# Kernel tuning notes

Measured on AMD Instinct MI355X. Metric: run time of the kernel, lower is better.

Reference implementation:

```python
import jax, jax.numpy as jnp
import numpy as np

IMG_SIZE = 1536.0
NUM_ANCHORS = 145152  # 3*(48^2 + 96^2 + 192^2) for strides 32/16/8 at 1536px
NUM_CH = 85           # 4 box + 1 obj + 80 classes


def setup_inputs() -> dict:
    key = jax.random.key(0)
    k1, k2 = jax.random.split(key)
    predictions = jax.random.uniform(k1, (1, NUM_ANCHORS, NUM_CH), dtype=jnp.float32)
    score_threshold = jax.random.uniform(k2, (1,), dtype=jnp.float32)
    return {"predictions": predictions, "score_threshold": score_threshold}


def _yolo2xywh(bboxes):
    # center-x/y + w/h -> corner-ish (x1, y1, x2, y2) as in the torch helper
    x = bboxes[..., 0] - bboxes[..., 2] / 2
    y = bboxes[..., 1] - bboxes[..., 3] / 2
    w = bboxes[..., 0] + bboxes[..., 2] / 2
    h = bboxes[..., 1] + bboxes[..., 3] / 2
    return jnp.stack((x, y, w, h), axis=2)


def reference(predictions, score_threshold):
    # threshold=False path: static shapes, no data-dependent compaction
    cls = predictions[..., 5:]
    class_conf = jnp.max(cls, axis=2, keepdims=True)           # [1, N, 1]
    class_pred = jnp.argmax(cls, axis=2, keepdims=True)        # [1, N, 1] int
    bboxes = predictions[..., :4] / IMG_SIZE                   # [1, N, 4]
    objectness = predictions[..., 4]                           # [1, N]
    scores = objectness * class_conf[..., 0]                   # [1, N]
    bboxes = _yolo2xywh(bboxes)                                # [1, N, 4]
    detections = jnp.concatenate(
        (bboxes, class_conf, class_pred.astype(jnp.float32)), axis=2)  # [1, N, 6]
    return (bboxes[0], scores[0], class_pred[0, :, 0], detections)
```

## Files before the change

### kernel.cpp

```cpp
#include <hip/hip_runtime.h>


#define N_ANCH 145152
#define NCH 85
#define NCLS 80

constexpr float INV_IMG = 1.0f / 1536.0f;
constexpr int TPB = 256;

__global__ __launch_bounds__(TPB)
void yolo_decode(const float* __restrict__ pred, float* __restrict__ out) {
    const int a = blockIdx.x * TPB + threadIdx.x;
    const float* __restrict__ p = pred + (size_t)a * NCH;

    float4 cls[20];
    #pragma unroll
    for (int j = 0; j < 20; ++j)
        cls[j] = *(const float4*)(p + 5 + 4 * j);
    const float4 bb = *(const float4*)(p);
    const float obj = p[4];

    float cmax = cls[0].x;
    int cidx = 0;
    #pragma unroll
    for (int j = 0; j < 20; ++j) {
        const float v0 = cls[j].x, v1 = cls[j].y, v2 = cls[j].z, v3 = cls[j].w;
        const int k = 4 * j;
        if (v0 > cmax) { cmax = v0; cidx = k;     }
        if (v1 > cmax) { cmax = v1; cidx = k + 1; }
        if (v2 > cmax) { cmax = v2; cidx = k + 2; }
        if (v3 > cmax) { cmax = v3; cidx = k + 3; }
    }

    const float cx = bb.x * INV_IMG;
    const float cy = bb.y * INV_IMG;
    const float hw = bb.z * (INV_IMG * 0.5f);
    const float hh = bb.w * (INV_IMG * 0.5f);
    const float x0 = cx - hw, y0 = cy - hh;
    const float x1 = cx + hw, y1 = cy + hh;

    const float score = obj * cmax;
    const float clsf  = (float)cidx;

    ((float4*)out)[a] = make_float4(x0, y0, x1, y1);
    out[4 * N_ANCH + a] = score;
    out[5 * N_ANCH + a] = clsf;
    float2* det = (float2*)(out + 6 * (size_t)N_ANCH + (size_t)a * 6);
    det[0] = make_float2(x0, y0);
    det[1] = make_float2(x1, y1);
    det[2] = make_float2(cmax, clsf);
}

extern "C" void kernel_launch(void* const* d_in, const int* in_sizes, int n_in,
                              void* d_out, int out_size, void* d_ws, size_t ws_size,
                              hipStream_t stream) {
    const float* pred = (const float*)d_in[0];
    float* out = (float*)d_out;
    yolo_decode<<<N_ANCH / TPB, TPB, 0, stream>>>(pred, out);
}
```

Baseline: 89.89 us.

## Assign 16 lanes per anchor with coalesced loads and shuffle argmax

Each anchor's 85 channels are now read cooperatively by a 16-lane group, so consecutive lanes load consecutive floats instead of each thread reading a strided 340-byte row. The class max/argmax is computed per lane and then reduced with xor shuffles, breaking ties toward the lower index. Output stores are split across lanes. This adds shuffle and launch overhead and leaves many lanes idle during the stores.

```diff
diff --git a/kernel.cpp b/kernel.cpp
--- a/kernel.cpp
+++ b/kernel.cpp
@@ -1,54 +1,71 @@
 #include <hip/hip_runtime.h>
+#include <float.h>
 
 
 #define N_ANCH 145152
 #define NCH 85
-#define NCLS 80
 
 constexpr float INV_IMG = 1.0f / 1536.0f;
 constexpr int TPB = 256;
+constexpr int GRP = 16;
+constexpr int APB = TPB / GRP;
 
 __global__ __launch_bounds__(TPB)
 void yolo_decode(const float* __restrict__ pred, float* __restrict__ out) {
-    const int a = blockIdx.x * TPB + threadIdx.x;
+    const int t  = threadIdx.x;
+    const int li = t & (GRP - 1);
+    const int a  = blockIdx.x * APB + (t >> 4);
     const float* __restrict__ p = pred + (size_t)a * NCH;
 
-    float4 cls[20];
+    const float r0 = p[li];
+    const float r1 = p[li + 16];
+    const float r2 = p[li + 32];
+    const float r3 = p[li + 48];
+    const float r4 = p[li + 64];
+    const float r5 = (li < 5) ? p[li + 80] : -FLT_MAX;
+
+    const float bx  = __shfl(r0, 0, GRP);
+    const float by  = __shfl(r0, 1, GRP);
+    const float bw  = __shfl(r0, 2, GRP);
+    const float bh  = __shfl(r0, 3, GRP);
+    const float obj = __shfl(r0, 4, GRP);
+
+    float v = (li >= 5) ? r0 : -FLT_MAX;
+    int   c = li - 5;
+    if (r1 > v) { v = r1; c = li + 11; }
+    if (r2 > v) { v = r2; c = li + 27; }
+    if (r3 > v) { v = r3; c = li + 43; }
+    if (r4 > v) { v = r4; c = li + 59; }
+    if (r5 > v) { v = r5; c = li + 75; }
+
     #pragma unroll
-    for (int j = 0; j < 20; ++j)
-        cls[j] = *(const float4*)(p + 5 + 4 * j);
-    const float4 bb = *(const float4*)(p);
-    const float obj = p[4];
-
-    float cmax = cls[0].x;
-    int cidx = 0;
-    #pragma unroll
-    for (int j = 0; j < 20; ++j) {
-        const float v0 = cls[j].x, v1 = cls[j].y, v2 = cls[j].z, v3 = cls[j].w;
-        const int k = 4 * j;
-        if (v0 > cmax) { cmax = v0; cidx = k;     }
-        if (v1 > cmax) { cmax = v1; cidx = k + 1; }
-        if (v2 > cmax) { cmax = v2; cidx = k + 2; }
-        if (v3 > cmax) { cmax = v3; cidx = k + 3; }
+    for (int m = 8; m >= 1; m >>= 1) {
+        const float ov = __shfl_xor(v, m);
+        const int   oc = __shfl_xor(c, m);
+        if (ov > v || (ov == v && oc < c)) { v = ov; c = oc; }
     }
 
-    const float cx = bb.x * INV_IMG;
-    const float cy = bb.y * INV_IMG;
-    const float hw = bb.z * (INV_IMG * 0.5f);
-    const float hh = bb.w * (INV_IMG * 0.5f);
+    const float cx = bx * INV_IMG;
+    const float cy = by * INV_IMG;
+    const float hw = bw * (INV_IMG * 0.5f);
+    const float hh = bh * (INV_IMG * 0.5f);
     const float x0 = cx - hw, y0 = cy - hh;
     const float x1 = cx + hw, y1 = cy + hh;
+    const float score = obj * v;
+    const float clsf  = (float)c;
 
-    const float score = obj * cmax;
-    const float clsf  = (float)cidx;
-
-    ((float4*)out)[a] = make_float4(x0, y0, x1, y1);
-    out[4 * N_ANCH + a] = score;
-    out[5 * N_ANCH + a] = clsf;
-    float2* det = (float2*)(out + 6 * (size_t)N_ANCH + (size_t)a * 6);
-    det[0] = make_float2(x0, y0);
-    det[1] = make_float2(x1, y1);
-    det[2] = make_float2(cmax, clsf);
+    if (li == 0) {
+        ((float4*)out)[a] = make_float4(x0, y0, x1, y1);
+    } else if (li == 1) {
+        out[4 * N_ANCH + a] = score;
+    } else if (li == 2) {
+        out[5 * N_ANCH + a] = clsf;
+    } else if (li < 6) {
+        float2* det = (float2*)(out + 6 * (size_t)N_ANCH + (size_t)a * 6);
+        if      (li == 3) det[0] = make_float2(x0, y0);
+        else if (li == 4) det[1] = make_float2(x1, y1);
+        else              det[2] = make_float2(v, clsf);
+    }
 }
 
 extern "C" void kernel_launch(void* const* d_in, const int* in_sizes, int n_in,
@@ -56,5 +73,5 @@
                               hipStream_t stream) {
     const float* pred = (const float*)d_in[0];
     float* out = (float*)d_out;
-    yolo_decode<<<N_ANCH / TPB, TPB, 0, stream>>>(pred, out);
+    yolo_decode<<<N_ANCH / APB, TPB, 0, stream>>>(pred, out);
 }
```

Result: faster. 84.11 us (-6.4%).
